# Kernel tuning notes

Measured on AMD Instinct MI355X. Metric: run time of the kernel, lower is better.

## Reference

```python
import jax, jax.numpy as jnp
import numpy as np

SIZE = (128.0, 128.0, 128.0)
FEATURE_BLOCK_IDS = (1, 2, 3)


def _trilerp(feat, coords, power):
    # feat: [B, D, H, W, C]; coords: [B, N, 3] in [0, 1]
    B = coords.shape[0]
    scale = jnp.asarray([0.5 ** power * SIZE[0],
                         0.5 ** power * SIZE[1],
                         0.5 ** power * SIZE[2]], dtype=coords.dtype)
    hi = float(min(feat.shape[1:4])) - 1.01
    idx = jnp.clip(coords * scale, 0.01, hi)  # [B, N, 3]
    ix, iy, iz = idx[..., 0], idx[..., 1], idx[..., 2]
    x1, x2 = jnp.floor(ix), jnp.ceil(ix)
    y1, y2 = jnp.floor(iy), jnp.ceil(iy)
    z1, z2 = jnp.floor(iz), jnp.ceil(iz)
    b = jnp.arange(B)[:, None]  # broadcast batch index

    def g(xi, yi, zi):
        return feat[b, xi.astype(jnp.int32), yi.astype(jnp.int32), zi.astype(jnp.int32)]

    wx, wx2 = (ix - x1)[..., None], (x2 - ix)[..., None]
    wy, wy2 = (iy - y1)[..., None], (y2 - iy)[..., None]
    wz, wz2 = (iz - z1)[..., None], (z2 - iz)[..., None]

    # z = z1 plane
    lerp_x1 = g(x2, y1, z1) * wx + g(x1, y1, z1) * wx2
    lerp_x2 = g(x2, y2, z1) * wx + g(x1, y2, z1) * wx2
    lerp_y1 = lerp_x2 * wy + lerp_x1 * wy2
    # z = z2 plane
    lerp_x1 = g(x2, y1, z2) * wx + g(x1, y1, z2) * wx2
    lerp_x2 = g(x2, y2, z2) * wx + g(x1, y2, z2) * wx2
    lerp_y2 = lerp_x2 * wy + lerp_x1 * wy2
    return lerp_y2 * wz + lerp_y1 * wz2  # [B, N, C]


def setup_inputs() -> dict:
    key = jax.random.key(0)
    ks = jax.random.split(key, 7)
    B, N = 2, 50000
    return {
        'features0': jax.random.normal(ks[0], (B, 128, 128, 128, 1), jnp.float32),
        'features1': jax.random.normal(ks[1], (B, 64, 64, 64, 32), jnp.float32),
        'features2': jax.random.normal(ks[2], (B, 32, 32, 32, 64), jnp.float32),
        'features3': jax.random.normal(ks[3], (B, 16, 16, 16, 128), jnp.float32),
        'features4': jax.random.normal(ks[4], (B, 8, 8, 8, 256), jnp.float32),
        'mesh_coords': jax.random.uniform(ks[5], (B, N, 3), jnp.float32),
        'mesh_features': jax.random.normal(ks[6], (B, N, 3), jnp.float32),
    }


def reference(features0, features1, features2, features3, features4, mesh_coords, mesh_features):
    feats = [features0, features1, features2, features3, features4]
    # mesh_coords is [B, N, 3] -> one coord group, reshape is identity
    sampled = [_trilerp(feats[i], mesh_coords, i) for i in FEATURE_BLOCK_IDS]
    out = jnp.concatenate(sampled, axis=-1)
    return jnp.concatenate([out, mesh_features], axis=-1)
```

## Files before the change

kernel.cpp:

```cpp
#include <hip/hip_runtime.h>


__global__ __launch_bounds__(256) void trilerp_kernel(
    const float* __restrict__ f1,
    const float* __restrict__ f2,
    const float* __restrict__ f3,
    const float* __restrict__ coords,
    const float* __restrict__ meshf,
    float* __restrict__ out,
    int nPts)
{
    const int pt = blockIdx.x;
    const int t  = threadIdx.x;
    if (t >= 227) return;

    float* o = out + (size_t)pt * 227;

    if (t >= 224) {
        o[t] = meshf[(size_t)pt * 3 + (t - 224)];
        return;
    }

    const int b = pt / nPts;

    const float cx = coords[(size_t)pt * 3 + 0];
    const float cy = coords[(size_t)pt * 3 + 1];
    const float cz = coords[(size_t)pt * 3 + 2];

    const float* feat;
    int D, C, c;
    if (t < 32)       { feat = f1; D = 64; C = 32;  c = t;      }
    else if (t < 96)  { feat = f2; D = 32; C = 64;  c = t - 32; }
    else              { feat = f3; D = 16; C = 128; c = t - 96; }

    const float scale = (float)D;
    const float hi    = (float)((double)D - 1.01);

    float ix = fminf(fmaxf(cx * scale, 0.01f), hi);
    float iy = fminf(fmaxf(cy * scale, 0.01f), hi);
    float iz = fminf(fmaxf(cz * scale, 0.01f), hi);

    const float x1f = floorf(ix), x2f = ceilf(ix);
    const float y1f = floorf(iy), y2f = ceilf(iy);
    const float z1f = floorf(iz), z2f = ceilf(iz);
    const int x1 = (int)x1f, x2 = (int)x2f;
    const int y1 = (int)y1f, y2 = (int)y2f;
    const int z1 = (int)z1f, z2 = (int)z2f;

    const float wx = ix - x1f, wx2 = x2f - ix;
    const float wy = iy - y1f, wy2 = y2f - iy;
    const float wz = iz - z1f, wz2 = z2f - iz;

    const size_t base = (size_t)b * D * D * D * C + c;
    #define OFF(X, Y, Z) (base + (size_t)((((X) * D + (Y)) * D + (Z))) * C)

    const float v111 = feat[OFF(x1, y1, z1)];
    const float v211 = feat[OFF(x2, y1, z1)];
    const float v121 = feat[OFF(x1, y2, z1)];
    const float v221 = feat[OFF(x2, y2, z1)];
    const float v112 = feat[OFF(x1, y1, z2)];
    const float v212 = feat[OFF(x2, y1, z2)];
    const float v122 = feat[OFF(x1, y2, z2)];
    const float v222 = feat[OFF(x2, y2, z2)];
    #undef OFF

    const float lx1a = v211 * wx + v111 * wx2;
    const float lx2a = v221 * wx + v121 * wx2;
    const float ly1  = lx2a * wy + lx1a * wy2;
    const float lx1b = v212 * wx + v112 * wx2;
    const float lx2b = v222 * wx + v122 * wx2;
    const float ly2  = lx2b * wy + lx1b * wy2;

    o[t] = ly2 * wz + ly1 * wz2;
}

extern "C" void kernel_launch(void* const* d_in, const int* in_sizes, int n_in,
                              void* d_out, int out_size, void* d_ws, size_t ws_size,
                              hipStream_t stream) {
    const float* f1     = (const float*)d_in[1];
    const float* f2     = (const float*)d_in[2];
    const float* f3     = (const float*)d_in[3];
    const float* coords = (const float*)d_in[5];
    const float* meshf  = (const float*)d_in[6];
    float* out = (float*)d_out;

    const int B = in_sizes[1] / (64 * 64 * 64 * 32);
    const int N = in_sizes[5] / (B * 3);

    trilerp_kernel<<<dim3(B * N), dim3(256), 0, stream>>>(
        f1, f2, f3, coords, meshf, out, N);
}
```

Before: 258.0 us.

## Map one wavefront per point with float4 channel gathers and nontemporal stores

Restructures the launch so that each 64-lane wavefront handles one point, packing four points per 256-thread block instead of one point per block. Each lane gathers float4 vectors of four channels per corner, which cuts the number of load instructions and the number of idle threads. Output is written with scalar nontemporal stores, because the row stride of 227 floats leaves rows unaligned for float4 stores. Index math drops to 32-bit ints, which is safe for these sizes but could overflow on larger inputs.

```diff
diff --git a/kernel.cpp b/kernel.cpp
--- a/kernel.cpp
+++ b/kernel.cpp
@@ -8,37 +8,38 @@
     const float* __restrict__ coords,
     const float* __restrict__ meshf,
     float* __restrict__ out,
-    int nPts)
+    int N)
 {
-    const int pt = blockIdx.x;
-    const int t  = threadIdx.x;
-    if (t >= 227) return;
+    const int lane = threadIdx.x & 63;
+    const int wv   = threadIdx.x >> 6;
+    const int pn   = blockIdx.x * 4 + wv;
+    if (pn >= N) return;
+    const int b  = blockIdx.y;
+    const int pt = b * N + pn;
 
-    float* o = out + (size_t)pt * 227;
-
-    if (t >= 224) {
-        o[t] = meshf[(size_t)pt * 3 + (t - 224)];
+    if (lane >= 56) {
+        if (lane < 59) {
+            __builtin_nontemporal_store(meshf[pt * 3 + (lane - 56)],
+                                        &out[pt * 227 + 224 + (lane - 56)]);
+        }
         return;
     }
 
-    const int b = pt / nPts;
+    const float cx = coords[pt * 3 + 0];
+    const float cy = coords[pt * 3 + 1];
+    const float cz = coords[pt * 3 + 2];
 
-    const float cx = coords[(size_t)pt * 3 + 0];
-    const float cy = coords[(size_t)pt * 3 + 1];
-    const float cz = coords[(size_t)pt * 3 + 2];
-
-    const float* feat;
-    int D, C, c;
-    if (t < 32)       { feat = f1; D = 64; C = 32;  c = t;      }
-    else if (t < 96)  { feat = f2; D = 32; C = 64;  c = t - 32; }
-    else              { feat = f3; D = 16; C = 128; c = t - 96; }
+    const float4* fp; int D, C4, c4, oc;
+    if (lane < 8)       { fp = (const float4*)f1; D = 64; C4 = 8;  c4 = lane * 4;        oc = c4;      }
+    else if (lane < 24) { fp = (const float4*)f2; D = 32; C4 = 16; c4 = (lane - 8) * 4;  oc = 32 + c4; }
+    else                { fp = (const float4*)f3; D = 16; C4 = 32; c4 = (lane - 24) * 4; oc = 96 + c4; }
 
     const float scale = (float)D;
     const float hi    = (float)((double)D - 1.01);
 
-    float ix = fminf(fmaxf(cx * scale, 0.01f), hi);
-    float iy = fminf(fmaxf(cy * scale, 0.01f), hi);
-    float iz = fminf(fmaxf(cz * scale, 0.01f), hi);
+    const float ix = fminf(fmaxf(cx * scale, 0.01f), hi);
+    const float iy = fminf(fmaxf(cy * scale, 0.01f), hi);
+    const float iz = fminf(fmaxf(cz * scale, 0.01f), hi);
 
     const float x1f = floorf(ix), x2f = ceilf(ix);
     const float y1f = floorf(iy), y2f = ceilf(iy);
@@ -51,27 +52,62 @@
     const float wy = iy - y1f, wy2 = y2f - iy;
     const float wz = iz - z1f, wz2 = z2f - iz;
 
-    const size_t base = (size_t)b * D * D * D * C + c;
-    #define OFF(X, Y, Z) (base + (size_t)((((X) * D + (Y)) * D + (Z))) * C)
+    const int base4 = b * (D * D * D * C4) + (c4 >> 2);
+    #define IDX(X, Y, Z) (base4 + (((X) * D + (Y)) * D + (Z)) * C4)
 
-    const float v111 = feat[OFF(x1, y1, z1)];
-    const float v211 = feat[OFF(x2, y1, z1)];
-    const float v121 = feat[OFF(x1, y2, z1)];
-    const float v221 = feat[OFF(x2, y2, z1)];
-    const float v112 = feat[OFF(x1, y1, z2)];
-    const float v212 = feat[OFF(x2, y1, z2)];
-    const float v122 = feat[OFF(x1, y2, z2)];
-    const float v222 = feat[OFF(x2, y2, z2)];
-    #undef OFF
+    const float4 v111 = fp[IDX(x1, y1, z1)];
+    const float4 v211 = fp[IDX(x2, y1, z1)];
+    const float4 v121 = fp[IDX(x1, y2, z1)];
+    const float4 v221 = fp[IDX(x2, y2, z1)];
+    const float4 v112 = fp[IDX(x1, y1, z2)];
+    const float4 v212 = fp[IDX(x2, y1, z2)];
+    const float4 v122 = fp[IDX(x1, y2, z2)];
+    const float4 v222 = fp[IDX(x2, y2, z2)];
+    #undef IDX
 
-    const float lx1a = v211 * wx + v111 * wx2;
-    const float lx2a = v221 * wx + v121 * wx2;
-    const float ly1  = lx2a * wy + lx1a * wy2;
-    const float lx1b = v212 * wx + v112 * wx2;
-    const float lx2b = v222 * wx + v122 * wx2;
-    const float ly2  = lx2b * wy + lx1b * wy2;
+    float4 r;
+    {
+        const float lx1a = v211.x * wx + v111.x * wx2;
+        const float lx2a = v221.x * wx + v121.x * wx2;
+        const float ly1  = lx2a * wy + lx1a * wy2;
+        const float lx1b = v212.x * wx + v112.x * wx2;
+        const float lx2b = v222.x * wx + v122.x * wx2;
+        const float ly2  = lx2b * wy + lx1b * wy2;
+        r.x = ly2 * wz + ly1 * wz2;
+    }
+    {
+        const float lx1a = v211.y * wx + v111.y * wx2;
+        const float lx2a = v221.y * wx + v121.y * wx2;
+        const float ly1  = lx2a * wy + lx1a * wy2;
+        const float lx1b = v212.y * wx + v112.y * wx2;
+        const float lx2b = v222.y * wx + v122.y * wx2;
+        const float ly2  = lx2b * wy + lx1b * wy2;
+        r.y = ly2 * wz + ly1 * wz2;
+    }
+    {
+        const float lx1a = v211.z * wx + v111.z * wx2;
+        const float lx2a = v221.z * wx + v121.z * wx2;
+        const float ly1  = lx2a * wy + lx1a * wy2;
+        const float lx1b = v212.z * wx + v112.z * wx2;
+        const float lx2b = v222.z * wx + v122.z * wx2;
+        const float ly2  = lx2b * wy + lx1b * wy2;
+        r.z = ly2 * wz + ly1 * wz2;
+    }
+    {
+        const float lx1a = v211.w * wx + v111.w * wx2;
+        const float lx2a = v221.w * wx + v121.w * wx2;
+        const float ly1  = lx2a * wy + lx1a * wy2;
+        const float lx1b = v212.w * wx + v112.w * wx2;
+        const float lx2b = v222.w * wx + v122.w * wx2;
+        const float ly2  = lx2b * wy + lx1b * wy2;
+        r.w = ly2 * wz + ly1 * wz2;
+    }
 
-    o[t] = ly2 * wz + ly1 * wz2;
+    float* o = out + pt * 227 + oc;
+    __builtin_nontemporal_store(r.x, o + 0);
+    __builtin_nontemporal_store(r.y, o + 1);
+    __builtin_nontemporal_store(r.z, o + 2);
+    __builtin_nontemporal_store(r.w, o + 3);
 }
 
 extern "C" void kernel_launch(void* const* d_in, const int* in_sizes, int n_in,
@@ -87,6 +123,6 @@
     const int B = in_sizes[1] / (64 * 64 * 64 * 32);
     const int N = in_sizes[5] / (B * 3);
 
-    trilerp_kernel<<<dim3(B * N), dim3(256), 0, stream>>>(
+    trilerp_kernel<<<dim3((N + 3) / 4, B), dim3(256), 0, stream>>>(
         f1, f2, f3, coords, meshf, out, N);
 }
```

Measured after the change: 217.1 us. 1.19x faster.

## Bucket-sort points spatially and gather float4 channels, two points per wavefront

Applied to the files above, without the earlier changes.

Adds a counting-sort pre-pass (histogram, scan, scatter into 8x8x8 buckets per batch) so that points processed together touch nearby voxels, which should improve L2 locality of the gathers. The main kernel now handles two points per 64-lane wavefront and loads features as float4, four channels per lane, instead of one block per point with scalar loads. Output stores become nontemporal. The cost is four extra small kernel launches and atomics on every call, plus output writes scattered in sorted order.

```diff
diff --git a/kernel.cpp b/kernel.cpp
--- a/kernel.cpp
+++ b/kernel.cpp
@@ -1,77 +1,185 @@
 #include <hip/hip_runtime.h>
 
 
-__global__ __launch_bounds__(256) void trilerp_kernel(
+#define BUCK_AXIS 8
+#define BUCK_PER_BATCH 512
+#define MAX_BUCKETS 1024
+
+__device__ __forceinline__ int point_batch(int p, int N) {
+    int b = 0;
+    while (p >= N) { p -= N; ++b; }
+    return b;
+}
+
+__device__ __forceinline__ int bucket_key(const float* __restrict__ coords,
+                                          int t, int N) {
+    const float cx = coords[t * 3 + 0];
+    const float cy = coords[t * 3 + 1];
+    const float cz = coords[t * 3 + 2];
+    int kx = (int)(cx * (float)BUCK_AXIS);
+    int ky = (int)(cy * (float)BUCK_AXIS);
+    int kz = (int)(cz * (float)BUCK_AXIS);
+    kx = min(max(kx, 0), BUCK_AXIS - 1);
+    ky = min(max(ky, 0), BUCK_AXIS - 1);
+    kz = min(max(kz, 0), BUCK_AXIS - 1);
+    const int b = point_batch(t, N);
+    return b * BUCK_PER_BATCH + ((kx << 6) | (ky << 3) | kz);
+}
+
+__global__ void zero_kernel(int* __restrict__ hist, int n) {
+    const int t = blockIdx.x * blockDim.x + threadIdx.x;
+    if (t < n) hist[t] = 0;
+}
+
+__global__ void hist_kernel(const float* __restrict__ coords,
+                            int* __restrict__ hist, int N, int P) {
+    const int t = blockIdx.x * blockDim.x + threadIdx.x;
+    if (t >= P) return;
+    atomicAdd(&hist[bucket_key(coords, t, N)], 1);
+}
+
+__global__ __launch_bounds__(MAX_BUCKETS) void scan_kernel(
+    const int* __restrict__ hist, int* __restrict__ ofs, int n) {
+    __shared__ int tmp[MAX_BUCKETS];
+    const int t = threadIdx.x;
+    const int v = (t < n) ? hist[t] : 0;
+    tmp[t] = v;
+    __syncthreads();
+    for (int s = 1; s < MAX_BUCKETS; s <<= 1) {
+        const int add = (t >= s) ? tmp[t - s] : 0;
+        __syncthreads();
+        tmp[t] += add;
+        __syncthreads();
+    }
+    if (t < n) ofs[t] = tmp[t] - v;
+}
+
+__global__ void scatter_kernel(const float* __restrict__ coords,
+                               int* __restrict__ ofs, int* __restrict__ perm,
+                               int N, int P) {
+    const int t = blockIdx.x * blockDim.x + threadIdx.x;
+    if (t >= P) return;
+    const int key = bucket_key(coords, t, N);
+    const int b   = key >= BUCK_PER_BATCH;
+    const int idx = atomicAdd(&ofs[key], 1);
+    perm[idx] = t | (b << 28);
+}
+
+__device__ __forceinline__ float4 lerpw(const float4 a, const float4 b,
+                                        float w, float w2) {
+    float4 r;
+    r.x = a.x * w + b.x * w2;
+    r.y = a.y * w + b.y * w2;
+    r.z = a.z * w + b.z * w2;
+    r.w = a.w * w + b.w * w2;
+    return r;
+}
+
+__global__ __launch_bounds__(256) void trilerp_main(
     const float* __restrict__ f1,
     const float* __restrict__ f2,
     const float* __restrict__ f3,
     const float* __restrict__ coords,
     const float* __restrict__ meshf,
     float* __restrict__ out,
-    int nPts)
+    const int* __restrict__ perm,
+    int N, int P)
 {
-    const int pt = blockIdx.x;
-    const int t  = threadIdx.x;
-    if (t >= 227) return;
-
-    float* o = out + (size_t)pt * 227;
-
-    if (t >= 224) {
-        o[t] = meshf[(size_t)pt * 3 + (t - 224)];
+    const int lane = threadIdx.x & 63;
+    const int w    = (blockIdx.x * 256 + threadIdx.x) >> 6;
+    const int i0   = w * 2;
+    if (i0 >= P) return;
+    const bool has1 = (i0 + 1) < P;
+
+    int pts[2], bs[2];
+    if (perm) {
+        const int e0 = perm[i0];
+        const int e1 = has1 ? perm[i0 + 1] : e0;
+        pts[0] = e0 & 0x0FFFFFFF;  bs[0] = e0 >> 28;
+        pts[1] = e1 & 0x0FFFFFFF;  bs[1] = e1 >> 28;
+    } else {
+        pts[0] = i0;                       bs[0] = point_batch(pts[0], N);
+        pts[1] = has1 ? (i0 + 1) : i0;     bs[1] = point_batch(pts[1], N);
+    }
+
+    if (lane >= 56) {
+        const int i = lane - 56;
+        if (i < 6) {
+            const int pi = i / 3;
+            const int ch = i - pi * 3;
+            if (pi == 0 || has1) {
+                const int p = pts[pi];
+                __builtin_nontemporal_store(meshf[p * 3 + ch],
+                                            &out[p * 227 + 224 + ch]);
+            }
+        }
         return;
     }
 
-    const int b = pt / nPts;
-
-    const float cx = coords[(size_t)pt * 3 + 0];
-    const float cy = coords[(size_t)pt * 3 + 1];
-    const float cz = coords[(size_t)pt * 3 + 2];
-
-    const float* feat;
-    int D, C, c;
-    if (t < 32)       { feat = f1; D = 64; C = 32;  c = t;      }
-    else if (t < 96)  { feat = f2; D = 32; C = 64;  c = t - 32; }
-    else              { feat = f3; D = 16; C = 128; c = t - 96; }
+    const float4* fp; int D, C4, c4g, oc;
+    if (lane < 8)       { fp = (const float4*)f1; D = 64; C4 = 8;  c4g = lane;      oc = lane * 4;             }
+    else if (lane < 24) { fp = (const float4*)f2; D = 32; C4 = 16; c4g = lane - 8;  oc = 32 + (lane - 8) * 4;  }
+    else                { fp = (const float4*)f3; D = 16; C4 = 32; c4g = lane - 24; oc = 96 + (lane - 24) * 4; }
 
     const float scale = (float)D;
     const float hi    = (float)((double)D - 1.01);
-
-    float ix = fminf(fmaxf(cx * scale, 0.01f), hi);
-    float iy = fminf(fmaxf(cy * scale, 0.01f), hi);
-    float iz = fminf(fmaxf(cz * scale, 0.01f), hi);
-
-    const float x1f = floorf(ix), x2f = ceilf(ix);
-    const float y1f = floorf(iy), y2f = ceilf(iy);
-    const float z1f = floorf(iz), z2f = ceilf(iz);
-    const int x1 = (int)x1f, x2 = (int)x2f;
-    const int y1 = (int)y1f, y2 = (int)y2f;
-    const int z1 = (int)z1f, z2 = (int)z2f;
-
-    const float wx = ix - x1f, wx2 = x2f - ix;
-    const float wy = iy - y1f, wy2 = y2f - iy;
-    const float wz = iz - z1f, wz2 = z2f - iz;
-
-    const size_t base = (size_t)b * D * D * D * C + c;
-    #define OFF(X, Y, Z) (base + (size_t)((((X) * D + (Y)) * D + (Z))) * C)
-
-    const float v111 = feat[OFF(x1, y1, z1)];
-    const float v211 = feat[OFF(x2, y1, z1)];
-    const float v121 = feat[OFF(x1, y2, z1)];
-    const float v221 = feat[OFF(x2, y2, z1)];
-    const float v112 = feat[OFF(x1, y1, z2)];
-    const float v212 = feat[OFF(x2, y1, z2)];
-    const float v122 = feat[OFF(x1, y2, z2)];
-    const float v222 = feat[OFF(x2, y2, z2)];
-    #undef OFF
-
-    const float lx1a = v211 * wx + v111 * wx2;
-    const float lx2a = v221 * wx + v121 * wx2;
-    const float ly1  = lx2a * wy + lx1a * wy2;
-    const float lx1b = v212 * wx + v112 * wx2;
-    const float lx2b = v222 * wx + v122 * wx2;
-    const float ly2  = lx2b * wy + lx1b * wy2;
-
-    o[t] = ly2 * wz + ly1 * wz2;
+    const int   vol4  = D * D * D * C4;
+
+    float4 v[2][8];
+    float wxa[2], wxb[2], wya[2], wyb[2], wza[2], wzb[2];
+
+    #pragma unroll
+    for (int q = 0; q < 2; ++q) {
+        const int p = pts[q];
+        const float cx = coords[p * 3 + 0];
+        const float cy = coords[p * 3 + 1];
+        const float cz = coords[p * 3 + 2];
+
+        const float ix = fminf(fmaxf(cx * scale, 0.01f), hi);
+        const float iy = fminf(fmaxf(cy * scale, 0.01f), hi);
+        const float iz = fminf(fmaxf(cz * scale, 0.01f), hi);
+
+        const float x1f = floorf(ix), x2f = ceilf(ix);
+        const float y1f = floorf(iy), y2f = ceilf(iy);
+        const float z1f = floorf(iz), z2f = ceilf(iz);
+        const int x1 = (int)x1f, x2 = (int)x2f;
+        const int y1 = (int)y1f, y2 = (int)y2f;
+        const int z1 = (int)z1f, z2 = (int)z2f;
+
+        wxa[q] = ix - x1f; wxb[q] = x2f - ix;
+        wya[q] = iy - y1f; wyb[q] = y2f - iy;
+        wza[q] = iz - z1f; wzb[q] = z2f - iz;
+
+        const int base4 = bs[q] * vol4 + c4g;
+        #define IDX(X, Y, Z) (base4 + (((X) * D + (Y)) * D + (Z)) * C4)
+        v[q][0] = fp[IDX(x1, y1, z1)];
+        v[q][1] = fp[IDX(x2, y1, z1)];
+        v[q][2] = fp[IDX(x1, y2, z1)];
+        v[q][3] = fp[IDX(x2, y2, z1)];
+        v[q][4] = fp[IDX(x1, y1, z2)];
+        v[q][5] = fp[IDX(x2, y1, z2)];
+        v[q][6] = fp[IDX(x1, y2, z2)];
+        v[q][7] = fp[IDX(x2, y2, z2)];
+        #undef IDX
+    }
+
+    #pragma unroll
+    for (int q = 0; q < 2; ++q) {
+        if (q == 1 && !has1) break;
+        const float4 lx1a = lerpw(v[q][1], v[q][0], wxa[q], wxb[q]);
+        const float4 lx2a = lerpw(v[q][3], v[q][2], wxa[q], wxb[q]);
+        const float4 ly1  = lerpw(lx2a,    lx1a,    wya[q], wyb[q]);
+        const float4 lx1b = lerpw(v[q][5], v[q][4], wxa[q], wxb[q]);
+        const float4 lx2b = lerpw(v[q][7], v[q][6], wxa[q], wxb[q]);
+        const float4 ly2  = lerpw(lx2b,    lx1b,    wya[q], wyb[q]);
+        const float4 r    = lerpw(ly2,     ly1,     wza[q], wzb[q]);
+
+        float* o = out + pts[q] * 227 + oc;
+        __builtin_nontemporal_store(r.x, o + 0);
+        __builtin_nontemporal_store(r.y, o + 1);
+        __builtin_nontemporal_store(r.z, o + 2);
+        __builtin_nontemporal_store(r.w, o + 3);
+    }
 }
 
 extern "C" void kernel_launch(void* const* d_in, const int* in_sizes, int n_in,
@@ -86,7 +194,22 @@
 
     const int B = in_sizes[1] / (64 * 64 * 64 * 32);
     const int N = in_sizes[5] / (B * 3);
-
-    trilerp_kernel<<<dim3(B * N), dim3(256), 0, stream>>>(
-        f1, f2, f3, coords, meshf, out, N);
-}
+    const int P = B * N;
+
+    int* hist = (int*)d_ws;
+    int* ofs  = hist + MAX_BUCKETS;
+    int* perm = hist + 2 * MAX_BUCKETS;
+    const size_t need = (size_t)(2 * MAX_BUCKETS + P) * sizeof(int);
+    const int nb = B * BUCK_PER_BATCH;
+    const bool useSort = (ws_size >= need) && (nb <= MAX_BUCKETS);
+
+    if (useSort) {
+        zero_kernel<<<dim3((nb + 255) / 256), dim3(256), 0, stream>>>(hist, nb);
+        hist_kernel<<<dim3((P + 255) / 256), dim3(256), 0, stream>>>(coords, hist, N, P);
+        scan_kernel<<<dim3(1), dim3(MAX_BUCKETS), 0, stream>>>(hist, ofs, nb);
+        scatter_kernel<<<dim3((P + 255) / 256), dim3(256), 0, stream>>>(coords, ofs, perm, N, P);
+    }
+
+    trilerp_main<<<dim3((P + 7) / 8), dim3(256), 0, stream>>>(
+        f1, f2, f3, coords, meshf, out, useSort ? perm : nullptr, N, P);
+}
```

Result: faster. 252.6 us (-2.1%).
